# Kernel optimization log

Measured on AMD Instinct MI355X. Metric: run time of the kernel, lower is better.

Reference implementation:

```python
import jax, jax.numpy as jnp
import numpy as np

EPS = 1e-5
C = 256
K = 3
K2 = K * K


def conv2d(x, w, b=None, groups=1):
    out = jax.lax.conv_general_dilated(
        x, w, (1, 1), 'VALID',
        dimension_numbers=('NCHW', 'OIHW', 'NCHW'),
        feature_group_count=groups)
    if b is not None:
        out = out + b[None, :, None, None]
    return out


def _bilinear_one(img, py, px):
    # img: [C,H,W]; py,px: [K2,ho,wo] float sampling coords (zero outside)
    _, H, W = img.shape
    y0 = jnp.floor(py)
    x0 = jnp.floor(px)
    dy = py - y0
    dx = px - x0
    y0i = y0.astype(jnp.int32)
    x0i = x0.astype(jnp.int32)

    def gather(yi, xi):
        valid = ((yi >= 0) & (yi < H) & (xi >= 0) & (xi < W)).astype(img.dtype)
        yc = jnp.clip(yi, 0, H - 1)
        xc = jnp.clip(xi, 0, W - 1)
        return img[:, yc, xc] * valid[None]  # [C,K2,ho,wo]

    w00 = (1 - dy) * (1 - dx)
    w01 = (1 - dy) * dx
    w10 = dy * (1 - dx)
    w11 = dy * dx
    return (gather(y0i, x0i) * w00[None] + gather(y0i, x0i + 1) * w01[None]
            + gather(y0i + 1, x0i) * w10[None] + gather(y0i + 1, x0i + 1) * w11[None])


def deform_conv(x, off_w, off_b, w, b):
    # ModulatedDeformConvPack: 3x3, stride=1, pad=0, dil=1, deformable_groups=1
    B, Cin, H, W = x.shape
    ho, wo = H - 2, W - 2
    om = conv2d(x, off_w, off_b)  # [B, 3*K2, ho, wo]
    o1, o2, m = om[:, :K2], om[:, K2:2 * K2], om[:, 2 * K2:]
    offset = jnp.concatenate([o1, o2], axis=1)  # [B, 2*K2, ho, wo]
    off_y = offset[:, 0::2]  # kernel reads y at channel 2k
    off_x = offset[:, 1::2]  # and x at channel 2k+1
    mask = jax.nn.sigmoid(m)  # [B,K2,ho,wo]
    ky, kx = jnp.meshgrid(jnp.arange(K), jnp.arange(K), indexing='ij')
    base_y = (ky.reshape(K2, 1, 1) + jnp.arange(ho).reshape(1, ho, 1)).astype(x.dtype)
    base_x = (kx.reshape(K2, 1, 1) + jnp.arange(wo).reshape(1, 1, wo)).astype(x.dtype)
    py = base_y[None] + off_y
    px = base_x[None] + off_x
    samples = jax.vmap(_bilinear_one)(x, py, px)  # [B,C,K2,ho,wo]
    samples = samples * mask[:, None]
    out = jnp.einsum('bckhw,ock->bohw', samples, w.reshape(w.shape[0], Cin, K2))
    return out + b[None, :, None, None]


def bn(x, g, b_, m, v):
    scale = g / jnp.sqrt(v + EPS)
    return (x - m[None, :, None, None]) * scale[None, :, None, None] + b_[None, :, None, None]


def xcorr(inst, exam):
    # batch-as-groups depthwise cross-correlation
    B = exam.shape[0]
    w = exam.reshape(B * C, 1, 18, 18)
    x = inst.reshape(1, B * C, 30, 30)
    out = jax.lax.conv_general_dilated(
        x, w, (1, 1), 'VALID',
        dimension_numbers=('NCHW', 'OIHW', 'NCHW'),
        feature_group_count=B * C)
    return out.reshape(B, C, 13, 13)


def _forward(examplar, instance, off_w, off_b, dcn_w, dcn_b,
             bn1_g, bn1_b, bn1_m, bn1_v,
             fus_w, fus_b, bn2_g, bn2_b, bn2_m, bn2_v,
             cls_w, cls_b, box_w, box_b):
    def head(x, i):  # deform conv + BN (eval)
        y = deform_conv(x, off_w[i], off_b[i], dcn_w[i], dcn_b[i])
        return bn(y, bn1_g[i], bn1_b[i], bn1_m[i], bn1_v[i])

    exam_cls = head(examplar, 0)
    inst_cls = head(instance, 1)
    exam_reg = head(examplar, 2)
    inst_reg = head(instance, 3)

    xc_cls = xcorr(inst_cls, exam_cls)
    xc_reg = xcorr(inst_reg, exam_reg)

    def fuse(x, i):  # 1x1 conv + BN + ReLU
        y = jnp.einsum('bchw,oc->bohw', x, fus_w[i]) + fus_b[i][None, :, None, None]
        return jax.nn.relu(bn(y, bn2_g[i], bn2_b[i], bn2_m[i], bn2_v[i]))

    f_cls = fuse(xc_cls, 0)
    f_reg = fuse(xc_reg, 1)

    cls_pred = jnp.einsum('bchw,oc->bohw', f_cls, cls_w) + cls_b[None, :, None, None]
    box_pred = jnp.einsum('bchw,oc->bohw', f_reg, box_w) + box_b[None, :, None, None]
    return cls_pred, box_pred


def setup_inputs() -> dict:
    key = jax.random.key(0)
    ks = jax.random.split(key, 24)
    B = 16
    d = {
        'examplar': jax.random.normal(ks[0], (B, C, 20, 20), jnp.float32),
        'instance': jax.random.normal(ks[1], (B, C, 32, 32), jnp.float32),
        # 4 deform heads: 0=exam_cls, 1=inst_cls, 2=exam_reg, 3=inst_reg
        'off_w': jax.random.normal(ks[2], (4, 3 * K2, C, K, K), jnp.float32) * 0.01,
        'off_b': jax.random.normal(ks[3], (4, 3 * K2), jnp.float32) * 0.01,
        'dcn_w': jax.random.normal(ks[4], (4, C, C, K, K), jnp.float32) * 0.05,
        'dcn_b': jax.random.normal(ks[5], (4, C), jnp.float32) * 0.05,
        'bn1_g': jax.random.uniform(ks[6], (4, C), jnp.float32) + 0.5,
        'bn1_b': jax.random.normal(ks[7], (4, C), jnp.float32) * 0.1,
        'bn1_m': jax.random.normal(ks[8], (4, C), jnp.float32) * 0.1,
        'bn1_v': jax.random.uniform(ks[9], (4, C), jnp.float32) + 0.5,
        # 2 fusion modules: 0=cls, 1=reg
        'fus_w': jax.random.normal(ks[10], (2, C, C), jnp.float32) * 0.05,
        'fus_b': jax.random.normal(ks[11], (2, C), jnp.float32) * 0.05,
        'bn2_g': jax.random.uniform(ks[12], (2, C), jnp.float32) + 0.5,
        'bn2_b': jax.random.normal(ks[13], (2, C), jnp.float32) * 0.1,
        'bn2_m': jax.random.normal(ks[14], (2, C), jnp.float32) * 0.1,
        'bn2_v': jax.random.uniform(ks[15], (2, C), jnp.float32) + 0.5,
        'cls_w': jax.random.normal(ks[16], (4, C), jnp.float32) * 0.05,
        'cls_b': jax.random.normal(ks[17], (4,), jnp.float32) * 0.05,
        'box_w': jax.random.normal(ks[18], (16, C), jnp.float32) * 0.05,
        'box_b': jax.random.normal(ks[19], (16,), jnp.float32) * 0.05,
    }
    return d


def reference(examplar, instance, off_w, off_b, dcn_w, dcn_b,
              bn1_g, bn1_b, bn1_m, bn1_v,
              fus_w, fus_b, bn2_g, bn2_b, bn2_m, bn2_v,
              cls_w, cls_b, box_w, box_b):
    return _forward(examplar, instance, off_w, off_b, dcn_w, dcn_b,
                    bn1_g, bn1_b, bn1_m, bn1_v,
                    fus_w, fus_b, bn2_g, bn2_b, bn2_m, bn2_v,
                    cls_w, cls_b, box_w, box_b)
```

## Files before the change

kernel.cpp:

```cpp
#include <hip/hip_runtime.h>
#include <math.h>

#define EPSBN 1e-5f

typedef _Float16 f16x8 __attribute__((ext_vector_type(8)));
typedef float    f32x4 __attribute__((ext_vector_type(4)));

__device__ __forceinline__ f16x8 splat8(float v) {
  _Float16 h = (_Float16)v;
  return (f16x8){h, h, h, h, h, h, h, h};
}

static constexpr size_t XF_EX = 0;
static constexpr size_t XF_IN = 819200;
static constexpr size_t WPK   = 2916352;
static constexpr size_t OWPK  = 4096000;
static constexpr size_t FWT   = 4243456;
static constexpr size_t OM0   = 4374528;
static constexpr size_t OM1   = 4514496;
static constexpr size_t OM2   = 4903296;
static constexpr size_t OM3   = 5043264;
static constexpr size_t HOUT0 = 5432064;
static constexpr size_t HOUT1 = 6759168;
static constexpr size_t HOUT2 = 10445568;
static constexpr size_t HOUT3 = 11772672;
static constexpr size_t XCB   = 15459072;

__global__ __launch_bounds__(256) void k_transpose(const float* __restrict__ in,
                                                   _Float16* __restrict__ out,
                                                   int H, int W) {
  int y = blockIdx.x, b = blockIdx.y;
  __shared__ float tile[32][257];
  int t = threadIdx.x;
  int x = t & 31, cb = t >> 5;
  for (int c0 = 0; c0 < 256; c0 += 8) {
    int c = c0 + cb;
    if (x < W) tile[x][c] = in[(((size_t)b * 256 + c) * H + y) * W + x];
  }
  __syncthreads();
  for (int x2 = 0; x2 < W; ++x2)
    out[((((size_t)b * H + y) * W + x2) << 8) + t] = (_Float16)tile[x2][t];
}

__global__ __launch_bounds__(256) void k_wpack(const float* __restrict__ w,
                                               _Float16* __restrict__ wp) {
  int idx = blockIdx.x * 256 + threadIdx.x;
  if (idx >= 4 * 9 * 8 * 16 * 64 * 8) return;
  int e  = idx & 7;
  int l  = (idx >> 3) & 63;
  int ot = (idx >> 9) & 15;
  int cs = (idx >> 13) & 7;
  int ht = idx >> 16;
  int tap = ht % 9, h = ht / 9;
  int o = ot * 16 + (l & 15);
  int c = cs * 32 + 8 * (l >> 4) + e;
  wp[idx] = (_Float16)w[((size_t)((h * 256 + o) * 256 + c)) * 9 + tap];
}

__global__ __launch_bounds__(256) void k_owpack(const float* __restrict__ w,
                                                _Float16* __restrict__ wp) {
  int idx = blockIdx.x * 256 + threadIdx.x;
  if (idx >= 4 * 9 * 8 * 2 * 64 * 8) return;
  int e  = idx & 7;
  int l  = (idx >> 3) & 63;
  int ot = (idx >> 9) & 1;
  int cs = (idx >> 10) & 7;
  int ht = idx >> 13;
  int tap = ht % 9, h = ht / 9;
  int o = ot * 16 + (l & 15);
  int c = cs * 32 + 8 * (l >> 4) + e;
  wp[idx] = (o < 27) ? (_Float16)w[((size_t)((h * 27 + o) * 256 + c)) * 9 + tap]
                     : (_Float16)0.f;
}

__global__ __launch_bounds__(256) void k_fwt(const float* __restrict__ w,
                                             float* __restrict__ wt) {
  int idx = blockIdx.x * 256 + threadIdx.x;
  int o = idx & 255, c = (idx >> 8) & 255, i = idx >> 16;
  wt[idx] = w[(i << 16) + (o << 8) + c];
}

__global__ __launch_bounds__(256) void k_offmfma(const _Float16* __restrict__ xh_ex,
                                                 const _Float16* __restrict__ xh_in,
                                                 const _Float16* __restrict__ owpk,
                                                 const float* __restrict__ off_b,
                                                 float* __restrict__ ws) {
  const int h = blockIdx.z, b = blockIdx.y;
  const int HH[4] = {20, 32, 20, 32};
  const size_t OMO[4] = {OM0, OM1, OM2, OM3};
  const int H = HH[h], W = H, ho = H - 2, wo = W - 2, P = ho * wo;
  const int nblk = (P + 63) >> 6;
  if (blockIdx.x >= nblk) return;
  const int p0 = blockIdx.x << 6;
  const _Float16* xh = ((h & 1) ? xh_in : xh_ex) + (((size_t)b * H * W) << 8);

  __shared__ __align__(16) _Float16 S[64 * 256];
  __shared__ int rowoff[64];

  const int t = threadIdx.x, lane = t & 63, wave = t >> 6;
  if (t < 64) {
    int p = min(p0 + t, P - 1);
    int i = p / wo, j = p - i * wo;
    rowoff[t] = (i * W + j) << 8;
  }
  f32x4 acc0 = {0.f, 0.f, 0.f, 0.f}, acc1 = {0.f, 0.f, 0.f, 0.f};
  __syncthreads();

  const int o8 = t & 31;
  for (int tap = 0; tap < 9; ++tap) {
    const int ky = tap / 3, kx = tap - ky * 3;
    const int koff = (ky * W + kx) << 8;
    #pragma unroll
    for (int it = 0; it < 8; ++it) {
      int pl = it * 8 + (t >> 5);
      f16x8 v = *(const f16x8*)(xh + rowoff[pl] + koff + o8 * 8);
      *(f16x8*)((char*)S + pl * 512 + ((o8 * 16) ^ ((pl & 7) << 4))) = v;
    }
    __syncthreads();
    #pragma unroll
    for (int cs = 0; cs < 8; ++cs) {
      int ksg = tap * 8 + cs;
      const _Float16* ab = owpk + ((size_t)(h * 72 + ksg) * 2) * 512 + lane * 8;
      f16x8 a0 = *(const f16x8*)(ab);
      f16x8 a1 = *(const f16x8*)(ab + 512);
      int prow = wave * 16 + (lane & 15);
      f16x8 bf = *(const f16x8*)((char*)S + prow * 512 +
                                 ((cs * 64 + ((lane >> 4) << 4)) ^ ((prow & 7) << 4)));
      acc0 = __builtin_amdgcn_mfma_f32_16x16x32_f16(a0, bf, acc0, 0, 0, 0);
      acc1 = __builtin_amdgcn_mfma_f32_16x16x32_f16(a1, bf, acc1, 0, 0, 0);
    }
    __syncthreads();
  }
  float* om = ws + OMO[h] + (size_t)b * 27 * P;
  int p = p0 + wave * 16 + (lane & 15);
  if (p < P) {
    #pragma unroll
    for (int r = 0; r < 4; ++r) {
      int o = 4 * (lane >> 4) + r;
      if (o < 27) om[o * P + p] = acc0[r] + off_b[h * 27 + o];
      int o2 = o + 16;
      if (o2 < 27) om[o2 * P + p] = acc1[r] + off_b[h * 27 + o2];
    }
  }
}

__global__ __launch_bounds__(256) void k_dgemm(const _Float16* __restrict__ xh_ex,
                                               const _Float16* __restrict__ xh_in,
                                               const _Float16* __restrict__ wpk,
                                               float* __restrict__ ws,
                                               const float* __restrict__ dcn_b,
                                               const float* __restrict__ g1,
                                               const float* __restrict__ b1,
                                               const float* __restrict__ m1,
                                               const float* __restrict__ v1) {
  const int h = blockIdx.z;
  const int HH4[4] = {20, 32, 20, 32};
  const size_t OMO[4] = {OM0, OM1, OM2, OM3};
  const size_t HOO[4] = {HOUT0, HOUT1, HOUT2, HOUT3};
  const int H = HH4[h], W = H, ho = H - 2, wo = W - 2, P = ho * wo;
  const int nblk = (P + 63) >> 6;
  if (blockIdx.x >= nblk) return;
  const int b = blockIdx.y;
  const int p0 = blockIdx.x << 6;
  const _Float16* xh = (h & 1) ? xh_in : xh_ex;
  const float* om = ws + OMO[h] + (size_t)b * 27 * P;
  float* outp = ws + HOO[h] + (size_t)b * 256 * P;

  __shared__ float4 swt4[576];
  __shared__ int4   sad4[576];
  __shared__ __align__(16) _Float16 S[64 * 256];

  const int t = threadIdx.x, lane = t & 63, wave = t >> 6;

  for (int e = t; e < 576; e += 256) {
    int pl = e / 9, k = e - pl * 9;
    float w4[4] = {0.f, 0.f, 0.f, 0.f};
    int a4[4] = {0, 0, 0, 0};
    int p = p0 + pl;
    if (p < P) {
      int i = p / wo, j = p - i * wo;
      float oy = om[(2 * k) * P + p];
      float ox = om[(2 * k + 1) * P + p];
      float mm = om[(18 + k) * P + p];
      float msk = 1.f / (1.f + __expf(-mm));
      int ky = k / 3, kx = k - ky * 3;
      float py = (float)(ky + i) + oy;
      float px = (float)(kx + j) + ox;
      float fy = floorf(py), fx = floorf(px);
      int y0 = (int)fy, x0 = (int)fx;
      float dy = py - fy, dx = px - fx;
      #pragma unroll
      for (int q = 0; q < 4; ++q) {
        int yy = y0 + (q >> 1), xx = x0 + (q & 1);
        bool vld = (yy >= 0) && (yy < H) && (xx >= 0) && (xx < W);
        int yc = min(max(yy, 0), H - 1), xc = min(max(xx, 0), W - 1);
        float wq = ((q >> 1) ? dy : 1.f - dy) * ((q & 1) ? dx : 1.f - dx);
        w4[q] = vld ? wq * msk : 0.f;
        a4[q] = ((blockIdx.y * H + yc) * W + xc) << 8;
      }
    }
    swt4[e] = make_float4(w4[0], w4[1], w4[2], w4[3]);
    sad4[e] = make_int4(a4[0], a4[1], a4[2], a4[3]);
  }

  f32x4 acc[4][4];
  #pragma unroll
  for (int a = 0; a < 4; ++a)
    #pragma unroll
    for (int n = 0; n < 4; ++n) acc[a][n] = (f32x4){0.f, 0.f, 0.f, 0.f};

  __syncthreads();

  const int o8 = t & 31;
  for (int tap = 0; tap < 9; ++tap) {
    #pragma unroll
    for (int it = 0; it < 8; ++it) {
      int pl = it * 8 + (t >> 5);
      float4 w4 = swt4[pl * 9 + tap];
      int4   a4 = sad4[pl * 9 + tap];
      const _Float16* xb = xh + o8 * 8;
      f16x8 x0 = *(const f16x8*)(xb + a4.x);
      f16x8 x1 = *(const f16x8*)(xb + a4.y);
      f16x8 x2 = *(const f16x8*)(xb + a4.z);
      f16x8 x3 = *(const f16x8*)(xb + a4.w);
      f16x8 s = x0 * splat8(w4.x) + x1 * splat8(w4.y) + x2 * splat8(w4.z) + x3 * splat8(w4.w);
      *(f16x8*)((char*)S + pl * 512 + ((o8 * 16) ^ ((pl & 7) << 4))) = s;
    }
    __syncthreads();
    #pragma unroll
    for (int cs = 0; cs < 8; ++cs) {
      int ksg = tap * 8 + cs;
      const _Float16* ab = wpk + ((size_t)(h * 72 + ksg) * 16 + wave * 4) * 512 + lane * 8;
      f16x8 A0 = *(const f16x8*)(ab);
      f16x8 A1 = *(const f16x8*)(ab + 512);
      f16x8 A2 = *(const f16x8*)(ab + 1024);
      f16x8 A3 = *(const f16x8*)(ab + 1536);
      f16x8 B[4];
      #pragma unroll
      for (int n = 0; n < 4; ++n) {
        int prow = n * 16 + (lane & 15);
        B[n] = *(const f16x8*)((char*)S + prow * 512 +
                               ((cs * 64 + ((lane >> 4) << 4)) ^ ((prow & 7) << 4)));
      }
      #pragma unroll
      for (int n = 0; n < 4; ++n) {
        acc[0][n] = __builtin_amdgcn_mfma_f32_16x16x32_f16(A0, B[n], acc[0][n], 0, 0, 0);
        acc[1][n] = __builtin_amdgcn_mfma_f32_16x16x32_f16(A1, B[n], acc[1][n], 0, 0, 0);
        acc[2][n] = __builtin_amdgcn_mfma_f32_16x16x32_f16(A2, B[n], acc[2][n], 0, 0, 0);
        acc[3][n] = __builtin_amdgcn_mfma_f32_16x16x32_f16(A3, B[n], acc[3][n], 0, 0, 0);
      }
    }
    __syncthreads();
  }

  #pragma unroll
  for (int a = 0; a < 4; ++a) {
    int obase = (wave * 4 + a) * 16 + 4 * (lane >> 4);
    #pragma unroll
    for (int r = 0; r < 4; ++r) {
      int o = obase + r;
      float al = g1[h * 256 + o] * rsqrtf(v1[h * 256 + o] + EPSBN);
      float be = (dcn_b[h * 256 + o] - m1[h * 256 + o]) * al + b1[h * 256 + o];
      #pragma unroll
      for (int n = 0; n < 4; ++n) {
        int p = p0 + n * 16 + (lane & 15);
        if (p < P) outp[(size_t)o * P + p] = fmaf(acc[a][n][r], al, be);
      }
    }
  }
}

__global__ __launch_bounds__(192) void k_xcorr(float* __restrict__ ws) {
  int bc = blockIdx.x;
  int br = blockIdx.y;
  __shared__ float ex_s[324];
  __shared__ float in_s[900];
  const float* exb = ws + (br ? HOUT2 : HOUT0) + (size_t)bc * 324;
  const float* inb = ws + (br ? HOUT3 : HOUT1) + (size_t)bc * 900;
  int t = threadIdx.x;
  for (int idx = t; idx < 324; idx += 192) ex_s[idx] = exb[idx];
  for (int idx = t; idx < 900; idx += 192) in_s[idx] = inb[idx];
  __syncthreads();
  if (t < 169) {
    int i = t / 13, j = t - (t / 13) * 13;
    float acc = 0.f;
    for (int u = 0; u < 18; ++u) {
      const float* ir = in_s + (i + u) * 30 + j;
      const float* er = ex_s + u * 18;
      #pragma unroll 6
      for (int v = 0; v < 18; ++v) acc = fmaf(ir[v], er[v], acc);
    }
    ws[XCB + ((size_t)br * 4096 + bc) * 169 + t] = acc;
  }
}

__global__ __launch_bounds__(256) void k_fuse(float* __restrict__ ws,
                                              const float* __restrict__ fus_b,
                                              const float* __restrict__ g2,
                                              const float* __restrict__ b2,
                                              const float* __restrict__ m2,
                                              const float* __restrict__ v2,
                                              const float* __restrict__ ow,
                                              const float* __restrict__ ob,
                                              float* __restrict__ out,
                                              int n_out, int br) {
  int ij = blockIdx.x, b = blockIdx.y;
  int t = threadIdx.x;
  __shared__ float xv[256];
  __shared__ float fv[256];
  xv[t] = ws[XCB + ((size_t)br * 4096 + b * 256 + t) * 169 + ij];
  __syncthreads();
  const float* fwt = ws + FWT + ((size_t)br << 16);
  float acc = 0.f;
  for (int c = 0; c < 256; ++c) acc = fmaf(fwt[(c << 8) + t], xv[c], acc);
  float s2 = g2[t] * rsqrtf(v2[t] + EPSBN);
  float f = (acc + fus_b[t] - m2[t]) * s2 + b2[t];
  fv[t] = fmaxf(f, 0.f);
  __syncthreads();
  int w = t >> 6, lane = t & 63;
  for (int po = w; po < n_out; po += 4) {
    float part = 0.f;
    #pragma unroll
    for (int q = 0; q < 4; ++q)
      part += ow[(po << 8) + lane + (q << 6)] * fv[lane + (q << 6)];
    for (int off = 32; off; off >>= 1) part += __shfl_down(part, off);
    if (lane == 0) out[((size_t)b * n_out + po) * 169 + ij] = part + ob[po];
  }
}

extern "C" void kernel_launch(void* const* d_in, const int* in_sizes, int n_in,
                              void* d_out, int out_size, void* d_ws, size_t ws_size,
                              hipStream_t stream) {
  const float* ex    = (const float*)d_in[0];
  const float* inst  = (const float*)d_in[1];
  const float* off_w = (const float*)d_in[2];
  const float* off_b = (const float*)d_in[3];
  const float* dcn_w = (const float*)d_in[4];
  const float* dcn_b = (const float*)d_in[5];
  const float* bn1_g = (const float*)d_in[6];
  const float* bn1_b = (const float*)d_in[7];
  const float* bn1_m = (const float*)d_in[8];
  const float* bn1_v = (const float*)d_in[9];
  const float* fus_w = (const float*)d_in[10];
  const float* fus_b = (const float*)d_in[11];
  const float* bn2_g = (const float*)d_in[12];
  const float* bn2_b = (const float*)d_in[13];
  const float* bn2_m = (const float*)d_in[14];
  const float* bn2_v = (const float*)d_in[15];
  const float* cls_w = (const float*)d_in[16];
  const float* cls_b = (const float*)d_in[17];
  const float* box_w = (const float*)d_in[18];
  const float* box_b = (const float*)d_in[19];
  float* out = (float*)d_out;
  float* ws  = (float*)d_ws;

  _Float16* xh_ex = (_Float16*)(ws + XF_EX);
  _Float16* xh_in = (_Float16*)(ws + XF_IN);
  _Float16* wpk   = (_Float16*)(ws + WPK);
  _Float16* owpk  = (_Float16*)(ws + OWPK);

  k_transpose<<<dim3(20, 16), 256, 0, stream>>>(ex,   xh_ex, 20, 20);
  k_transpose<<<dim3(32, 16), 256, 0, stream>>>(inst, xh_in, 32, 32);
  k_wpack <<<9216, 256, 0, stream>>>(dcn_w, wpk);
  k_owpack<<<1152, 256, 0, stream>>>(off_w, owpk);
  k_fwt   <<<512, 256, 0, stream>>>(fus_w, ws + FWT);
  k_offmfma<<<dim3(15, 16, 4), 256, 0, stream>>>(xh_ex, xh_in, owpk, off_b, ws);
  k_dgemm<<<dim3(15, 16, 4), 256, 0, stream>>>(xh_ex, xh_in, wpk, ws,
                                               dcn_b, bn1_g, bn1_b, bn1_m, bn1_v);
  k_xcorr<<<dim3(4096, 2), 192, 0, stream>>>(ws);
  k_fuse<<<dim3(169, 16), 256, 0, stream>>>(ws, fus_b, bn2_g, bn2_b, bn2_m, bn2_v,
                                            cls_w, cls_b, out, 4, 0);
  k_fuse<<<dim3(169, 16), 256, 0, stream>>>(ws, fus_b + 256, bn2_g + 256, bn2_b + 256,
                                            bn2_m + 256, bn2_v + 256, box_w, box_b,
                                            out + 10816, 16, 1);
}
```

Measured before the change: 395.3 us.

## Rewrite xcorr to batch 16 channels per block with register row tiling

```diff
diff --git a/kernel.cpp b/kernel.cpp
--- a/kernel.cpp
+++ b/kernel.cpp
@@ -4,6 +4,7 @@
 #define EPSBN 1e-5f
 
 typedef _Float16 f16x8 __attribute__((ext_vector_type(8)));
+typedef _Float16 f16x2 __attribute__((ext_vector_type(2)));
 typedef float    f32x4 __attribute__((ext_vector_type(4)));
 
 __device__ __forceinline__ f16x8 splat8(float v) {
@@ -270,27 +271,57 @@
   }
 }
 
-__global__ __launch_bounds__(192) void k_xcorr(float* __restrict__ ws) {
-  int bc = blockIdx.x;
-  int br = blockIdx.y;
-  __shared__ float ex_s[324];
-  __shared__ float in_s[900];
-  const float* exb = ws + (br ? HOUT2 : HOUT0) + (size_t)bc * 324;
-  const float* inb = ws + (br ? HOUT3 : HOUT1) + (size_t)bc * 900;
-  int t = threadIdx.x;
-  for (int idx = t; idx < 324; idx += 192) ex_s[idx] = exb[idx];
-  for (int idx = t; idx < 900; idx += 192) in_s[idx] = inb[idx];
-  __syncthreads();
-  if (t < 169) {
-    int i = t / 13, j = t - (t / 13) * 13;
-    float acc = 0.f;
-    for (int u = 0; u < 18; ++u) {
-      const float* ir = in_s + (i + u) * 30 + j;
-      const float* er = ex_s + u * 18;
-      #pragma unroll 6
-      for (int v = 0; v < 18; ++v) acc = fmaf(ir[v], er[v], acc);
-    }
-    ws[XCB + ((size_t)br * 4096 + bc) * 169 + t] = acc;
+__global__ __launch_bounds__(256) void k_xcorr3(float* __restrict__ ws) {
+  const int br = blockIdx.y;
+  const int bc0 = blockIdx.x << 4;
+  const float* exg = ws + (br ? HOUT2 : HOUT0) + (size_t)bc0 * 324;
+  const float* ing = ws + (br ? HOUT3 : HOUT1) + (size_t)bc0 * 900;
+  __shared__ __align__(16) _Float16 exl[16 * 324];
+  __shared__ __align__(16) _Float16 inl[16 * 960];
+  const int t = threadIdx.x;
+  for (int idx = t; idx < 16 * 324; idx += 256)
+    exl[idx] = (_Float16)exg[idx];
+  for (int idx = t; idx < 16 * 960; idx += 256) {
+    int c = idx & 31;
+    int rr = idx >> 5;
+    inl[idx] = (c < 30) ? (_Float16)ing[rr * 30 + c] : (_Float16)0.f;
+  }
+  __syncthreads();
+  const int lane = t & 63, wave = t >> 6;
+  const int sub = lane / 13;
+  const int i = lane - sub * 13;
+  const bool active = sub < 4;
+  const int bcl = wave * 4 + (active ? sub : 0);
+  float acc[13];
+  #pragma unroll
+  for (int j = 0; j < 13; ++j) acc[j] = 0.f;
+  const _Float16* inb = inl + bcl * 960;
+  const _Float16* exb = exl + bcl * 324;
+  for (int u = 0; u < 18; ++u) {
+    float a[30];
+    const _Float16* rp = inb + (i + u) * 32;
+    #pragma unroll
+    for (int x = 0; x < 15; ++x) {
+      f16x2 pr = *(const f16x2*)(rp + 2 * x);
+      a[2 * x] = (float)pr[0]; a[2 * x + 1] = (float)pr[1];
+    }
+    float e[18];
+    const _Float16* ep = exb + u * 18;
+    #pragma unroll
+    for (int x = 0; x < 9; ++x) {
+      f16x2 pr = *(const f16x2*)(ep + 2 * x);
+      e[2 * x] = (float)pr[0]; e[2 * x + 1] = (float)pr[1];
+    }
+    #pragma unroll
+    for (int v = 0; v < 18; ++v)
+      #pragma unroll
+      for (int j = 0; j < 13; ++j)
+        acc[j] = fmaf(a[v + j], e[v], acc[j]);
+  }
+  if (active) {
+    float* o = ws + XCB + ((size_t)(br * 4096 + bc0 + bcl)) * 169 + i * 13;
+    #pragma unroll
+    for (int j = 0; j < 13; ++j) o[j] = acc[j];
   }
 }
 
@@ -367,7 +398,7 @@
   k_offmfma<<<dim3(15, 16, 4), 256, 0, stream>>>(xh_ex, xh_in, owpk, off_b, ws);
   k_dgemm<<<dim3(15, 16, 4), 256, 0, stream>>>(xh_ex, xh_in, wpk, ws,
                                                dcn_b, bn1_g, bn1_b, bn1_m, bn1_v);
-  k_xcorr<<<dim3(4096, 2), 192, 0, stream>>>(ws);
+  k_xcorr3<<<dim3(256, 2), 256, 0, stream>>>(ws);
   k_fuse<<<dim3(169, 16), 256, 0, stream>>>(ws, fus_b, bn2_g, bn2_b, bn2_m, bn2_v,
                                             cls_w, cls_b, out, 4, 0);
   k_fuse<<<dim3(169, 16), 256, 0, stream>>>(ws, fus_b + 256, bn2_g + 256, bn2_b + 256,
```

New measurement: 338.1 us. 1.17x faster.
